# Kernel tuning notes

Hardware: AMD Instinct MI355X
Metric: run time of the kernel (lower is better)

Reference implementation:

```python
import jax, jax.numpy as jnp
import numpy as np

DIM = 1024
NUM_EXPERTS = 4
NUM_HEADS = 16
MLP_RATIO = 4
B, N = 8, 1024
EPS = 1e-5


def layernorm(x, w, b):
    mu = jnp.mean(x, axis=-1, keepdims=True)
    var = jnp.mean(jnp.square(x - mu), axis=-1, keepdims=True)
    return (x - mu) * jax.lax.rsqrt(var + EPS) * w + b


def setup_inputs() -> dict:
    key = jax.random.key(0)
    ks = jax.random.split(key, 6)
    x = jax.random.normal(ks[0], (B, N, DIM), dtype=jnp.float32)
    expert_mask = jax.random.randint(ks[1], (B, N), 0, NUM_EXPERTS)
    expert_probs = jax.random.uniform(ks[2], (B, N), dtype=jnp.float32)
    expand_dim = 3 * DIM + MLP_RATIO * DIM
    expand_weight = jax.random.normal(ks[3], (expand_dim, DIM), dtype=jnp.float32) * 0.02
    mlp_bias = jnp.zeros((MLP_RATIO * DIM,), dtype=jnp.float32)
    contract_weight = jax.random.normal(ks[4], (2 * DIM, MLP_RATIO * DIM + DIM), dtype=jnp.float32) * 0.02
    contract_bias = jnp.zeros((2 * DIM,), dtype=jnp.float32)
    norm1_w = jnp.ones((DIM,), dtype=jnp.float32)
    norm1_b = jnp.zeros((DIM,), dtype=jnp.float32)
    norm2_w = jnp.ones((2 * DIM,), dtype=jnp.float32)
    norm2_b = jnp.zeros((2 * DIM,), dtype=jnp.float32)
    return {"x": x, "expert_probs": expert_probs, "expand_weight": expand_weight,
            "mlp_bias": mlp_bias, "contract_weight": contract_weight,
            "contract_bias": contract_bias, "norm1_w": norm1_w, "norm1_b": norm1_b,
            "norm2_w": norm2_w, "norm2_b": norm2_b, "expert_mask": expert_mask}


def reference(x, expert_probs, expand_weight, mlp_bias, contract_weight,
              contract_bias, norm1_w, norm1_b, norm2_w, norm2_b, expert_mask):
    dim = DIM
    # nested sub-dim per token: expert m uses first dim >> (E-1-m) features
    shift = NUM_EXPERTS - 1 - expert_mask                       # (B, N)
    d_in = dim // jnp.left_shift(1, shift)                      # (B, N)
    in_mask = (jnp.arange(dim)[None, None, :] < d_in[..., None]).astype(x.dtype)

    # fused expand bias: [mlp_bias, qkv_bias(=zeros since qkv_bias=False)]
    input_bias = jnp.concatenate([mlp_bias, jnp.zeros((3 * dim,), x.dtype)], axis=-1)

    xn = layernorm(x, norm1_w, norm1_b) * in_mask               # nested_linear_expand input masking
    y = jnp.einsum('bnd,ed->bne', xn, expand_weight) + input_bias  # (B, N, 7*dim)

    qkv, mlp_hidden = y[..., :3 * dim], y[..., 3 * dim:]
    q = qkv[..., :dim]
    kv = layernorm(qkv[..., dim:], norm2_w, norm2_b)            # (B, N, 2*dim)
    k, v = kv[..., :dim], kv[..., dim:]

    # multi-head attention
    dh = dim // NUM_HEADS
    scale = dh ** -0.5
    b, n = x.shape[0], x.shape[1]
    def heads(t):
        return t.reshape(b, n, NUM_HEADS, dh).transpose(0, 2, 1, 3)
    qh, kh, vh = heads(q), heads(k), heads(v)
    attn = jax.nn.softmax(jnp.einsum('bhqd,bhkd->bhqk', qh, kh) * scale, axis=-1)
    attn_output = jnp.einsum('bhqk,bhkd->bhqd', attn, vh).transpose(0, 2, 1, 3).reshape(b, n, dim)

    # nested_linear_contract: full matmul, then mask outputs beyond (2*dim)>>shift
    concat_in = jnp.concatenate([jax.nn.gelu(mlp_hidden, approximate=False), attn_output], axis=-1)
    cy = jnp.einsum('bnc,oc->bno', concat_in, contract_weight) + contract_bias  # (B, N, 2*dim)
    d_out = (2 * dim) // jnp.left_shift(1, shift)
    out_mask = (jnp.arange(2 * dim)[None, None, :] < d_out[..., None]).astype(x.dtype)
    cy = cy * out_mask + jnp.concatenate([x, x], axis=-1)       # residual.repeat(1,1,2)

    mlp_output, attn_out = cy[..., :dim], cy[..., dim:]
    return attn_out + expert_probs[..., None] * mlp_output
```

## Files before the change

### kernel.cpp

```cpp
#include <hip/hip_runtime.h>
#include <cmath>

#define NT    8192
#define DIM_  1024
#define EXP_  7168
#define CD_   5120
#define OD_   2048
#define MPAD  8704
#define NRT   68

typedef __attribute__((ext_vector_type(8))) short short8;
typedef __attribute__((ext_vector_type(4))) float f32x4;
typedef __attribute__((ext_vector_type(4))) unsigned short ushort4_t;

__device__ __forceinline__ unsigned short f2bf(float f) {
  union { float f; unsigned u; } v; v.f = f;
  return (unsigned short)((v.u + 0x7FFFu + ((v.u >> 16) & 1u)) >> 16);
}
__device__ __forceinline__ float bf2f(unsigned short u) {
  union { unsigned u; float f; } v; v.u = ((unsigned)u) << 16;
  return v.f;
}
__device__ __forceinline__ float fast_gelu(float x) {
  float y = 1.5957691216f * (x + 0.044715f * x * x * x);
  float e = __expf(y);
  float t = 1.f - 2.f * __builtin_amdgcn_rcpf(1.f + e);
  return 0.5f * x * (1.f + t);
}

#define MFMA16(a, b, c) __builtin_amdgcn_mfma_f32_16x16x32_bf16(a, b, c, 0, 0, 0)

__global__ __launch_bounds__(256) void count_experts(const int* __restrict__ em,
                                                     int* __restrict__ blockCnt) {
  __shared__ int h[4];
  int tid = threadIdx.x;
  if (tid < 4) h[tid] = 0;
  __syncthreads();
  atomicAdd(&h[em[blockIdx.x * 256 + tid]], 1);
  __syncthreads();
  if (tid < 4) blockCnt[blockIdx.x * 4 + tid] = h[tid];
}

__global__ void scan_make(const int* __restrict__ blockCnt, int* __restrict__ desc) {
  if (threadIdx.x != 0) return;
  int cnt[4] = {0, 0, 0, 0};
  for (int b = 0; b < 32; b++)
    for (int e = 0; e < 4; e++) cnt[e] += blockCnt[b * 4 + e];
  int base[4]; int acc = 0;
  for (int e = 0; e < 4; e++) { base[e] = acc; acc += ((cnt[e] + 127) >> 7) << 7; }
  for (int e = 0; e < 4; e++) { desc[e] = base[e]; desc[4 + e] = cnt[e]; }
  for (int r = 0; r < NRT; r++) {
    int te = -1;
    for (int e = 0; e < 4; e++) {
      int lo = base[e] >> 7;
      int hi = (base[e] + (((cnt[e] + 127) >> 7) << 7)) >> 7;
      if (r >= lo && r < hi) te = e;
    }
    desc[8 + r] = te;
  }
  int run[4];
  for (int e = 0; e < 4; e++) run[e] = base[e];
  for (int b = 0; b < 32; b++)
    for (int e = 0; e < 4; e++) { desc[76 + b * 4 + e] = run[e]; run[e] += blockCnt[b * 4 + e]; }
}

__global__ __launch_bounds__(256) void fill_perm(int* __restrict__ perm) {
  int i = blockIdx.x * 256 + threadIdx.x;
  if (i < MPAD) perm[i] = -1;
}

__global__ __launch_bounds__(256) void scatter_perm(const int* __restrict__ em,
    const int* __restrict__ desc, int* __restrict__ perm, int* __restrict__ pos) {
  __shared__ int wsum[4][4];
  int tid = threadIdx.x;
  int wv = tid >> 6, ln = tid & 63;
  int t = blockIdx.x * 256 + tid;
  int e = em[t];
  int wrank = 0;
#pragma unroll
  for (int k = 0; k < 4; k++) {
    unsigned long long m = __ballot(e == k);
    if (ln == 0) wsum[wv][k] = __popcll(m);
    if (e == k) wrank = __popcll(m & ((1ull << ln) - 1ull));
  }
  __syncthreads();
  int off = desc[76 + blockIdx.x * 4 + e];
  for (int w = 0; w < wv; w++) off += wsum[w][e];
  int p = off + wrank;
  perm[p] = t;
  pos[t] = p;
}

__global__ __launch_bounds__(256) void cvt_bf16(const float* __restrict__ in,
                                                unsigned short* __restrict__ out, int n) {
  int i = (blockIdx.x * 256 + threadIdx.x) * 4;
  if (i >= n) return;
  float4 v = *(const float4*)(in + i);
  ushort4_t o;
  o[0] = f2bf(v.x); o[1] = f2bf(v.y); o[2] = f2bf(v.z); o[3] = f2bf(v.w);
  *(ushort4_t*)(out + i) = o;
}

__global__ __launch_bounds__(256) void ln1_kernel(const float* __restrict__ x,
    const float* __restrict__ w, const float* __restrict__ b,
    const int* __restrict__ emask, const int* __restrict__ pos,
    unsigned short* __restrict__ xn) {
  int wave = threadIdx.x >> 6, lane = threadIdx.x & 63;
  int t = blockIdx.x * 4 + wave;
  const float* xt = x + (size_t)t * DIM_;
  float4 v[4];
  float s = 0.f, s2 = 0.f;
#pragma unroll
  for (int i = 0; i < 4; i++) {
    v[i] = *(const float4*)(xt + i * 256 + lane * 4);
    s  += v[i].x + v[i].y + v[i].z + v[i].w;
    s2 += v[i].x * v[i].x + v[i].y * v[i].y + v[i].z * v[i].z + v[i].w * v[i].w;
  }
#pragma unroll
  for (int o = 1; o < 64; o <<= 1) { s += __shfl_xor(s, o); s2 += __shfl_xor(s2, o); }
  float mu = s * (1.f / 1024.f);
  float rs = rsqrtf(s2 * (1.f / 1024.f) - mu * mu + 1e-5f);
  int din = 1024 >> (3 - emask[t]);
  unsigned short* ot = xn + (size_t)pos[t] * DIM_;
#pragma unroll
  for (int i = 0; i < 4; i++) {
    int c0 = i * 256 + lane * 4;
    float fv[4] = { v[i].x, v[i].y, v[i].z, v[i].w };
    ushort4_t o;
#pragma unroll
    for (int j = 0; j < 4; j++) {
      int c = c0 + j;
      float val = (c < din) ? (fv[j] - mu) * rs * w[c] + b[c] : 0.f;
      o[j] = f2bf(val);
    }
    *(ushort4_t*)(ot + c0) = o;
  }
}

__global__ __launch_bounds__(256, 3) void gemm_grp1(
    const unsigned short* __restrict__ A, const unsigned short* __restrict__ W,
    const float* __restrict__ bias, const int* __restrict__ tdesc,
    const int* __restrict__ perm, unsigned short* __restrict__ out0,
    unsigned short* __restrict__ out1, unsigned short* __restrict__ out2) {
  __shared__ unsigned short lds[16384];
  unsigned short* As = lds;
  unsigned short* Bs = lds + 8192;
  const int r = blockIdx.y;
  const int e = tdesc[8 + r];
  if (e < 0) return;
  const int ntiles = 4 << e;
  constexpr int KK = 1024;

  const int tid = threadIdx.x;
  const int lane = tid & 63;
  const int wave = tid >> 6;
  const int wm = wave >> 1, wn = wave & 1;
  const int lg = lane >> 4, lr = lane & 15;

  constexpr int CPX = 56 >> 3;
  const int bx = (int)blockIdx.x;
  const int bn = (bx & 7) * CPX + (bx >> 3);
  const int n0 = bn * 128;
  const int m0 = r * 128;

  const int s0g = tid >> 3,        s1g = (256 + tid) >> 3;
  const int lc0 = (tid & 7) ^ (s0g & 7), lc1 = (tid & 7) ^ (s1g & 7);
  const int row0 = 2 * s0g + (lc0 >> 2), kc0 = lc0 & 3;
  const int row1 = 2 * s1g + (lc1 >> 2), kc1 = lc1 & 3;
  const unsigned short* aS0 = A + (size_t)(m0 + row0) * KK + kc0 * 8;
  const unsigned short* aS1 = A + (size_t)(m0 + row1) * KK + kc1 * 8;
  const unsigned short* bS0 = W + (size_t)(n0 + row0) * KK + kc0 * 8;
  const unsigned short* bS1 = W + (size_t)(n0 + row1) * KK + kc1 * 8;

#define GLD(SRC, DST)                                                                \
  __builtin_amdgcn_global_load_lds(                                                  \
      (const __attribute__((address_space(1))) void*)(SRC),                          \
      (__attribute__((address_space(3))) void*)(DST), 16, 0, 0)
#define STAGE(T, SLOT) {                                                             \
    GLD(aS0 + (size_t)(T) * 32, As + (SLOT) * 4096 + tid * 8);                       \
    GLD(aS1 + (size_t)(T) * 32, As + (SLOT) * 4096 + 2048 + tid * 8);                \
    GLD(bS0 + (size_t)(T) * 32, Bs + (SLOT) * 4096 + tid * 8);                       \
    GLD(bS1 + (size_t)(T) * 32, Bs + (SLOT) * 4096 + 2048 + tid * 8);                \
  }

  const int fb = (lr >> 1) * 128 + ((((lr & 1) << 2) + lg) ^ ((lr >> 1) & 7)) * 16;
  const char* apb = (const char*)As + wm * 4096 + fb;
  const char* bpb = (const char*)Bs + wn * 4096 + fb;

  short8 afr[4], bfr[4];
#define LDFRAG(C)                                                                    \
  _Pragma("unroll") for (int mi = 0; mi < 4; mi++)                                   \
    afr[mi] = *(const short8*)(apb + (C) * 8192 + mi * 1024);                        \
  _Pragma("unroll") for (int ni = 0; ni < 4; ni++)                                   \
    bfr[ni] = *(const short8*)(bpb + (C) * 8192 + ni * 1024);

  f32x4 acc[4][4];
  f32x4 zf = { 0.f, 0.f, 0.f, 0.f };
#pragma unroll
  for (int i = 0; i < 4; i++)
#pragma unroll
    for (int j = 0; j < 4; j++) acc[i][j] = zf;

  STAGE(0, 0)
  STAGE(1, 1)
  asm volatile("s_waitcnt vmcnt(4)" ::: "memory");
  __builtin_amdgcn_s_barrier();

#pragma unroll 1
  for (int t = 0; t < ntiles; ++t) {
    const int c = t & 1;
    LDFRAG(c)
    asm volatile("s_waitcnt lgkmcnt(0)" ::: "memory");
    __builtin_amdgcn_sched_barrier(0);
    __builtin_amdgcn_s_barrier();
    const int t2 = (t + 2 < ntiles) ? t + 2 : t;
    STAGE(t2, c)
    __builtin_amdgcn_s_setprio(1);
#pragma unroll
    for (int mi = 0; mi < 4; mi++)
#pragma unroll
      for (int ni = 0; ni < 4; ni++)
        acc[mi][ni] = MFMA16(afr[mi], bfr[ni], acc[mi][ni]);
    __builtin_amdgcn_s_setprio(0);
    asm volatile("s_waitcnt vmcnt(4)" ::: "memory");
    __builtin_amdgcn_s_barrier();
  }
  asm volatile("s_waitcnt vmcnt(0)" ::: "memory");

  const int n0w = n0 + wn * 64;
  auto epi_loop = [&](auto&& body) {
#pragma unroll
    for (int mi = 0; mi < 4; mi++)
#pragma unroll
      for (int ni = 0; ni < 4; ni++)
#pragma unroll
        for (int rr = 0; rr < 4; rr++) {
          int grow = m0 + wm * 64 + mi * 16 + lg * 4 + rr;
          int tk = perm[grow];
          int gcol = n0w + ni * 16 + lr;
          body(tk, gcol, acc[mi][ni][rr]);
        }
  };
  if (n0w < 1024) {
    epi_loop([&](int tk, int gcol, float v) {
      if (tk >= 0) {
        float vv = (v + bias[gcol]) * 0.125f;
        int bb = tk >> 10;
        int n = tk & 1023;
        int h = gcol >> 6;
        int d = gcol & 63;
        out0[(((size_t)(bb * 16 + h) * 1024 + n) << 6) + d] = f2bf(vv);
      }
    });
  } else if (n0w < 3072) {
    epi_loop([&](int tk, int gcol, float v) {
      if (tk >= 0) out1[(size_t)tk * OD_ + (gcol - 1024)] = f2bf(v + bias[gcol]);
    });
  } else {
    const bool hasb = (n0w < 4096);
    epi_loop([&](int tk, int gcol, float v) {
      if (tk >= 0) {
        float vb = v + (hasb ? bias[gcol] : 0.f);
        out2[(size_t)tk * CD_ + (gcol - 3072)] = f2bf(fast_gelu(vb));
      }
    });
  }
#undef GLD
#undef STAGE
#undef LDFRAG
}

__global__ __launch_bounds__(512, 2) void gemm2_8p(
    const unsigned short* __restrict__ A, const unsigned short* __restrict__ W,
    const float* __restrict__ bias, unsigned short* __restrict__ out0) {
  extern __shared__ unsigned short lds[];
  unsigned short* As = lds;
  unsigned short* Bs = lds + 32768;
  constexpr int KK = 5120;
  constexpr int NTILES = KK / 64;
  const int tid = threadIdx.x;
  const int lane = tid & 63;
  const int wave = tid >> 6;
  const int wm = wave >> 2;
  const int wn = wave & 3;
  const int lg = lane >> 4, lr = lane & 15;

  int cpx = (int)gridDim.x >> 3;
  int lid = ((int)blockIdx.x & 7) * cpx + ((int)blockIdx.x >> 3);
  int bm = lid >> 3, bn = lid & 7;
  int m0 = bm * 256, n0 = bn * 256;

  const int srow = tid >> 3;
  const int schunk = (tid & 7) ^ (srow & 7);
  const unsigned short* aSrc = A + (size_t)(m0 + srow) * KK + schunk * 8;
  const unsigned short* bSrc = W + (size_t)(n0 + srow) * KK + schunk * 8;

  const int xor0 = (lg ^ (lr & 7)) * 8;
  const int xor1 = ((4 + lg) ^ (lr & 7)) * 8;
  const unsigned short* ap0 = As + (wm * 64 + lr) * 64 + xor0;
  const unsigned short* ap1 = As + (wm * 64 + lr) * 64 + xor1;
  const unsigned short* bp0 = Bs + (wn * 32 + lr) * 64 + xor0;
  const unsigned short* bp1 = Bs + (wn * 32 + lr) * 64 + xor1;

#define STAGE_A(TT, SLOT, SEG)                                                       \
  __builtin_amdgcn_global_load_lds(                                                  \
    (const __attribute__((address_space(1))) void*)(aSrc +                           \
      (size_t)(SEG) * 64 * KK + (size_t)(TT) * 64),                                  \
    (__attribute__((address_space(3))) void*)(As + (SLOT) * 16384 +                  \
      (SEG) * 4096 + tid * 8), 16, 0, 0)
#define STAGE_B(TT, SLOT, SEG)                                                       \
  __builtin_amdgcn_global_load_lds(                                                  \
    (const __attribute__((address_space(1))) void*)(bSrc +                           \
      (size_t)(SEG) * 64 * KK + (size_t)(TT) * 64),                                  \
    (__attribute__((address_space(3))) void*)(Bs + (SLOT) * 16384 +                  \
      (SEG) * 4096 + tid * 8), 16, 0, 0)

  short8 afr[4][2], bfr[2][2][2];
#define LDFRAG_A(C, QM)                                                              \
  _Pragma("unroll") for (int mi = 0; mi < 4; mi++) {                                 \
    afr[mi][0] = *(const short8*)(ap0 + (C) * 16384 + (QM) * 8192 + mi * 1024);      \
    afr[mi][1] = *(const short8*)(ap1 + (C) * 16384 + (QM) * 8192 + mi * 1024);      \
  }
#define LDFRAG_B(C, QN)                                                              \
  _Pragma("unroll") for (int ni = 0; ni < 2; ni++) {                                 \
    bfr[QN][ni][0] = *(const short8*)(bp0 + (C) * 16384 + (QN) * 8192 + ni * 1024);  \
    bfr[QN][ni][1] = *(const short8*)(bp1 + (C) * 16384 + (QN) * 8192 + ni * 1024);  \
  }
#define DOMFMA(QM, QN)                                                               \
  __builtin_amdgcn_s_setprio(1);                                                     \
  _Pragma("unroll") for (int mi = 0; mi < 4; mi++)                                   \
  _Pragma("unroll") for (int ni = 0; ni < 2; ni++) {                                 \
    acc[(QM) * 4 + mi][(QN) * 2 + ni] =                                              \
        MFMA16(afr[mi][0], bfr[QN][ni][0], acc[(QM) * 4 + mi][(QN) * 2 + ni]);       \
    acc[(QM) * 4 + mi][(QN) * 2 + ni] =                                              \
        MFMA16(afr[mi][1], bfr[QN][ni][1], acc[(QM) * 4 + mi][(QN) * 2 + ni]);       \
  }                                                                                  \
  __builtin_amdgcn_s_setprio(0);

#define SCHED0 __builtin_amdgcn_sched_barrier(0)

#define TILE_BODY(T, C) {                                                            \
    const int tn1 = ((T) + 1 < NTILES) ? (T) + 1 : NTILES - 1;                       \
    const int tn2 = ((T) + 2 < NTILES) ? (T) + 2 : NTILES - 1;                       \
    LDFRAG_A(C, 0); LDFRAG_B(C, 0);                                                  \
    STAGE_B(tn1, (C) ^ 1, 2); STAGE_B(tn1, (C) ^ 1, 3);                              \
    SCHED0;                                                                          \
    __builtin_amdgcn_s_barrier();                                                    \
    asm volatile("s_waitcnt lgkmcnt(0)");                                            \
    SCHED0;                                                                          \
    DOMFMA(0, 0);                                                                    \
    asm volatile("s_waitcnt vmcnt(6)" ::: "memory");                                 \
    __builtin_amdgcn_s_barrier();                                                    \
    LDFRAG_B(C, 1);                                                                  \
    STAGE_A(tn1, (C) ^ 1, 2); STAGE_A(tn1, (C) ^ 1, 3);                              \
    SCHED0;                                                                          \
    __builtin_amdgcn_s_barrier();                                                    \
    asm volatile("s_waitcnt lgkmcnt(0)");                                            \
    SCHED0;                                                                          \
    DOMFMA(0, 1);                                                                    \
    __builtin_amdgcn_s_barrier();                                                    \
    LDFRAG_A(C, 1);                                                                  \
    STAGE_A(tn2, (C), 0); STAGE_A(tn2, (C), 1);                                      \
    SCHED0;                                                                          \
    __builtin_amdgcn_s_barrier();                                                    \
    asm volatile("s_waitcnt lgkmcnt(0)");                                            \
    SCHED0;                                                                          \
    DOMFMA(1, 0);                                                                    \
    __builtin_amdgcn_s_barrier();                                                    \
    STAGE_B(tn2, (C), 0); STAGE_B(tn2, (C), 1);                                      \
    SCHED0;                                                                          \
    __builtin_amdgcn_s_barrier();                                                    \
    DOMFMA(1, 1);                                                                    \
    asm volatile("s_waitcnt vmcnt(8)" ::: "memory");                                 \
    __builtin_amdgcn_s_barrier();                                                    \
  }

  f32x4 acc[8][4];
  f32x4 zf = { 0.f, 0.f, 0.f, 0.f };
#pragma unroll
  for (int i = 0; i < 8; i++)
#pragma unroll
    for (int j = 0; j < 4; j++) acc[i][j] = zf;

  STAGE_A(0, 0, 0); STAGE_A(0, 0, 1); STAGE_A(0, 0, 2); STAGE_A(0, 0, 3);
  STAGE_B(0, 0, 0); STAGE_B(0, 0, 1); STAGE_B(0, 0, 2); STAGE_B(0, 0, 3);
  STAGE_A(1, 1, 0); STAGE_A(1, 1, 1);
  STAGE_B(1, 1, 0); STAGE_B(1, 1, 1);
  asm volatile("s_waitcnt vmcnt(4)" ::: "memory");
  __builtin_amdgcn_s_barrier();

#pragma unroll 1
  for (int tp = 0; tp < NTILES / 2; ++tp) {
    TILE_BODY(2 * tp, 0)
    TILE_BODY(2 * tp + 1, 1)
  }
  asm volatile("s_waitcnt vmcnt(0)" ::: "memory");

#pragma unroll
  for (int mi8 = 0; mi8 < 8; mi8++) {
#pragma unroll
    for (int nj = 0; nj < 4; nj++) {
#pragma unroll
      for (int r = 0; r < 4; r++) {
        int grow = m0 + wm * 64 + (mi8 >> 2) * 128 + (mi8 & 3) * 16 + lg * 4 + r;
        int gcol = n0 + wn * 32 + (nj >> 1) * 128 + (nj & 1) * 16 + lr;
        float v = acc[mi8][nj][r] + bias[gcol];
        out0[(size_t)grow * OD_ + gcol] = f2bf(v);
      }
    }
  }
#undef STAGE_A
#undef STAGE_B
#undef LDFRAG_A
#undef LDFRAG_B
#undef DOMFMA
#undef SCHED0
#undef TILE_BODY
}

__global__ __launch_bounds__(256) void ln2_kernel(const unsigned short* __restrict__ kv,
    const float* __restrict__ w, const float* __restrict__ b,
    unsigned short* __restrict__ kb, unsigned short* __restrict__ vrm) {
  int wave = threadIdx.x >> 6, lane = threadIdx.x & 63;
  int t = blockIdx.x * 4 + wave;
  const unsigned short* p = kv + (size_t)t * OD_;
  float vals[4][8];
  float s = 0.f, s2 = 0.f;
#pragma unroll
  for (int i = 0; i < 4; i++) {
    short8 v = *(const short8*)(p + i * 512 + lane * 8);
#pragma unroll
    for (int j = 0; j < 8; j++) {
      float f = bf2f((unsigned short)v[j]);
      vals[i][j] = f; s += f; s2 += f * f;
    }
  }
#pragma unroll
  for (int o = 1; o < 64; o <<= 1) { s += __shfl_xor(s, o); s2 += __shfl_xor(s2, o); }
  float mu = s * (1.f / 2048.f);
  float rs = rsqrtf(s2 * (1.f / 2048.f) - mu * mu + 1e-5f);
  int bidx = t >> 10, n = t & 1023;
#pragma unroll
  for (int i = 0; i < 4; i++) {
    int c0 = i * 512 + lane * 8;
    short8 o8;
#pragma unroll
    for (int j = 0; j < 8; j++) {
      int c = c0 + j;
      o8[j] = (short)f2bf((vals[i][j] - mu) * rs * w[c] + b[c]);
    }
    if (c0 < 1024) {
      int h = c0 >> 6, d = c0 & 63;
      *(short8*)(kb + (((size_t)(bidx * 16 + h) * 1024 + n) << 6) + d) = o8;
    } else {
      *(short8*)(vrm + (size_t)t * 1024 + (c0 - 1024)) = o8;
    }
  }
}

__global__ __launch_bounds__(256) void transpose_v(const unsigned short* __restrict__ vrm,
                                                   unsigned short* __restrict__ vt) {
  int bh = blockIdx.x >> 4;
  int nblk = (blockIdx.x & 15) * 64;
  int b = bh >> 4, h = bh & 15;
  __shared__ unsigned short tile[64][65];
  int tid = threadIdx.x;
  int i = tid >> 2;
  int d0 = (tid & 3) * 16;
  const unsigned short* src = vrm + ((size_t)(b * 1024 + nblk + i)) * 1024 + h * 64 + d0;
  short8 v0 = *(const short8*)(src);
  short8 v1 = *(const short8*)(src + 8);
#pragma unroll
  for (int j = 0; j < 8; j++) {
    tile[d0 + j][i] = (unsigned short)v0[j];
    tile[d0 + 8 + j][i] = (unsigned short)v1[j];
  }
  __syncthreads();
  int d = tid >> 2;
  int i0 = (tid & 3) * 16;
  unsigned short* dst = vt + ((size_t)bh * 64 + d) * 1024 + nblk + i0;
  short8 o0, o1;
#pragma unroll
  for (int j = 0; j < 8; j++) { o0[j] = (short)tile[d][i0 + j]; o1[j] = (short)tile[d][i0 + 8 + j]; }
  *(short8*)dst = o0;
  *(short8*)(dst + 8) = o1;
}

__global__ __launch_bounds__(256) void attn_kernel(const unsigned short* __restrict__ q,
    const unsigned short* __restrict__ k, const unsigned short* __restrict__ vt,
    unsigned short* __restrict__ concat) {
  int bid = blockIdx.x;
  int bh = (bid & 7) + 8 * ((bid >> 3) & 15);
  int wv = threadIdx.x >> 6;
  int q0 = ((bid >> 7) & 7) * 128 + wv * 32;
  int lane = threadIdx.x & 63;
  int lg = lane >> 4, lr = lane & 15;
  __shared__ unsigned short plds[4][2][512];
  unsigned short* pw = &plds[wv][0][0];
  const unsigned short* qp = q + (size_t)bh * (1024 * 64);
  const unsigned short* kp = k + (size_t)bh * (1024 * 64);
  const unsigned short* vp = vt + (size_t)bh * (64 * 1024);
  short8 qf[2][2];
#pragma unroll
  for (int rb = 0; rb < 2; rb++)
#pragma unroll
    for (int c = 0; c < 2; c++)
      qf[rb][c] = *(const short8*)(qp + (q0 + rb * 16 + lr) * 64 + c * 32 + lg * 8);
  f32x4 zf = { 0.f, 0.f, 0.f, 0.f };
  f32x4 o[2][4];
  float m[2][4], l[2][4];
#pragma unroll
  for (int rb = 0; rb < 2; rb++) {
#pragma unroll
    for (int r = 0; r < 4; r++) { m[rb][r] = -1e30f; l[rb][r] = 0.f; }
#pragma unroll
    for (int nb = 0; nb < 4; nb++) o[rb][nb] = zf;
  }
  const int prd = lr * 32 + (((lg + lr) & 3) << 3);
  const unsigned short* kb0 = kp + (size_t)lr * 64 + lg * 8;
  const unsigned short* kb1 = kp + (size_t)(16 + lr) * 64 + lg * 8;
  const unsigned short* vb0 = vp + (size_t)(lr) * 1024 + lg * 8;
  const unsigned short* vb1 = vp + (size_t)(16 + lr) * 1024 + lg * 8;
  const unsigned short* vb2 = vp + (size_t)(32 + lr) * 1024 + lg * 8;
  const unsigned short* vb3 = vp + (size_t)(48 + lr) * 1024 + lg * 8;

  short8 kc0, kc1, kc2, kc3;
  short8 vc0, vc1, vc2, vc3;
  kc0 = *(const short8*)(kb0);
  kc1 = *(const short8*)(kb0 + 32);
  kc2 = *(const short8*)(kb1);
  kc3 = *(const short8*)(kb1 + 32);

#pragma unroll 1
  for (int kt = 0; kt < 1024; kt += 32) {
    vc0 = *(const short8*)(vb0 + kt);
    vc1 = *(const short8*)(vb1 + kt);
    vc2 = *(const short8*)(vb2 + kt);
    vc3 = *(const short8*)(vb3 + kt);
    asm volatile("s_waitcnt vmcnt(4)" ::: "memory");
    f32x4 s[2][2];
    s[0][0] = zf; s[0][1] = zf; s[1][0] = zf; s[1][1] = zf;
    __builtin_amdgcn_s_setprio(1);
    s[0][0] = MFMA16(qf[0][0], kc0, s[0][0]);
    s[0][0] = MFMA16(qf[0][1], kc1, s[0][0]);
    s[1][0] = MFMA16(qf[1][0], kc0, s[1][0]);
    s[1][0] = MFMA16(qf[1][1], kc1, s[1][0]);
    s[0][1] = MFMA16(qf[0][0], kc2, s[0][1]);
    s[0][1] = MFMA16(qf[0][1], kc3, s[0][1]);
    s[1][1] = MFMA16(qf[1][0], kc2, s[1][1]);
    s[1][1] = MFMA16(qf[1][1], kc3, s[1][1]);
    __builtin_amdgcn_s_setprio(0);
    {
      const size_t ktn = (kt + 32 < 1024) ? (size_t)(kt + 32) : (size_t)kt;
      kc0 = *(const short8*)(kb0 + ktn * 64);
      kc1 = *(const short8*)(kb0 + ktn * 64 + 32);
      kc2 = *(const short8*)(kb1 + ktn * 64);
      kc3 = *(const short8*)(kb1 + ktn * 64 + 32);
    }
#pragma unroll
    for (int rb = 0; rb < 2; rb++) {
      float lmax[4], rsum[4];
#pragma unroll
      for (int r = 0; r < 4; r++) lmax[r] = fmaxf(s[rb][0][r], s[rb][1][r]);
      bool loc = false;
#pragma unroll
      for (int r = 0; r < 4; r++) loc |= (lmax[r] > m[rb][r] + 8.f);
      if (__ballot(loc) != 0ull) {
        float mx[4];
#pragma unroll
        for (int r = 0; r < 4; r++) mx[r] = lmax[r];
#pragma unroll
        for (int ofs = 1; ofs < 16; ofs <<= 1)
#pragma unroll
          for (int r = 0; r < 4; r++) mx[r] = fmaxf(mx[r], __shfl_xor(mx[r], ofs));
#pragma unroll
        for (int r = 0; r < 4; r++) {
          float mn = fmaxf(m[rb][r], mx[r]);
          float al = __expf(m[rb][r] - mn);
          m[rb][r] = mn;
          l[rb][r] *= al;
#pragma unroll
          for (int nb = 0; nb < 4; nb++) o[rb][nb][r] *= al;
        }
      }
#pragma unroll
      for (int r = 0; r < 4; r++) {
        float p0 = __expf(s[rb][0][r] - m[rb][r]);
        float p1 = __expf(s[rb][1][r] - m[rb][r]);
        int q_ = lg * 4 + r;
        pw[rb * 512 + q_ * 32 + ((((lr >> 3) + q_) & 3) << 3) + (lr & 7)] = f2bf(p0);
        pw[rb * 512 + q_ * 32 + (((2 + (lr >> 3) + q_) & 3) << 3) + (lr & 7)] = f2bf(p1);
        rsum[r] = p0 + p1;
      }
#pragma unroll
      for (int ofs = 1; ofs < 16; ofs <<= 1)
#pragma unroll
        for (int r = 0; r < 4; r++) rsum[r] += __shfl_xor(rsum[r], ofs);
#pragma unroll
      for (int r = 0; r < 4; r++) l[rb][r] += rsum[r];
    }
    asm volatile("s_waitcnt lgkmcnt(0)" ::: "memory");
    short8 pf0 = *(const short8*)(pw + prd);
    short8 pf1 = *(const short8*)(pw + 512 + prd);
    asm volatile("s_waitcnt vmcnt(4)" ::: "memory");
    __builtin_amdgcn_s_setprio(1);
    o[0][0] = MFMA16(pf0, vc0, o[0][0]);
    o[1][0] = MFMA16(pf1, vc0, o[1][0]);
    o[0][1] = MFMA16(pf0, vc1, o[0][1]);
    o[1][1] = MFMA16(pf1, vc1, o[1][1]);
    o[0][2] = MFMA16(pf0, vc2, o[0][2]);
    o[1][2] = MFMA16(pf1, vc2, o[1][2]);
    o[0][3] = MFMA16(pf0, vc3, o[0][3]);
    o[1][3] = MFMA16(pf1, vc3, o[1][3]);
    __builtin_amdgcn_s_setprio(0);
  }
  int b = bh >> 4, h = bh & 15;
#pragma unroll
  for (int rb = 0; rb < 2; rb++)
#pragma unroll
    for (int r = 0; r < 4; r++) {
      int n = q0 + rb * 16 + lg * 4 + r;
      size_t t = (size_t)b * 1024 + n;
      float inv = 1.f / l[rb][r];
#pragma unroll
      for (int nb = 0; nb < 4; nb++)
        concat[t * CD_ + 4096 + h * 64 + nb * 16 + lr] = f2bf(o[rb][nb][r] * inv);
    }
}

__global__ __launch_bounds__(256) void final_epi(const unsigned short* __restrict__ cy,
    const float* __restrict__ x, const float* __restrict__ probs,
    const int* __restrict__ emask, float* __restrict__ out) {
  int t = blockIdx.x;
  int c = threadIdx.x * 4;
  int dout = 2048 >> (3 - emask[t]);
  float p = probs[t];
  const unsigned short* cyt = cy + (size_t)t * OD_;
  ushort4_t mv = *(const ushort4_t*)(cyt + c);
  ushort4_t av = *(const ushort4_t*)(cyt + 1024 + c);
  float4 xv = *(const float4*)(x + (size_t)t * 1024 + c);
  float xa[4] = { xv.x, xv.y, xv.z, xv.w };
  float4 o;
  float oa[4];
#pragma unroll
  for (int j = 0; j < 4; j++) {
    float mlp = ((c + j) < dout ? bf2f(mv[j]) : 0.f) + xa[j];
    float att = ((1024 + c + j) < dout ? bf2f(av[j]) : 0.f) + xa[j];
    oa[j] = att + p * mlp;
  }
  o.x = oa[0]; o.y = oa[1]; o.z = oa[2]; o.w = oa[3];
  *(float4*)(out + (size_t)t * 1024 + c) = o;
}

extern "C" void kernel_launch(void* const* d_in, const int* in_sizes, int n_in,
                              void* d_out, int out_size, void* d_ws, size_t ws_size,
                              hipStream_t stream) {
  const float* x        = (const float*)d_in[0];
  const float* probs    = (const float*)d_in[1];
  const float* we       = (const float*)d_in[2];
  const float* mlp_bias = (const float*)d_in[3];
  const float* wc       = (const float*)d_in[4];
  const float* cbias    = (const float*)d_in[5];
  const float* n1w      = (const float*)d_in[6];
  const float* n1b      = (const float*)d_in[7];
  const float* n2w      = (const float*)d_in[8];
  const float* n2b      = (const float*)d_in[9];
  const int*   emask    = (const int*)d_in[10];
  float* out = (float*)d_out;

  char* ws = (char*)d_ws;
  size_t off = 0;
  auto alloc = [&](size_t bytes) {
    char* p = ws + off;
    off += (bytes + 255) & ~(size_t)255;
    return p;
  };
  unsigned short* we_bf = (unsigned short*)alloc((size_t)EXP_ * DIM_ * 2);
  unsigned short* wc_bf = (unsigned short*)alloc((size_t)OD_ * CD_ * 2);
  unsigned short* xn    = (unsigned short*)alloc((size_t)MPAD * DIM_ * 2);
  unsigned short* qb    = (unsigned short*)alloc((size_t)NT * DIM_ * 2);
  unsigned short* kv    = (unsigned short*)alloc((size_t)NT * OD_ * 2);
  unsigned short* kb    = (unsigned short*)alloc((size_t)NT * DIM_ * 2);
  unsigned short* vt    = (unsigned short*)alloc((size_t)NT * DIM_ * 2);
  unsigned short* cc    = (unsigned short*)alloc((size_t)NT * CD_ * 2);
  int* blockCnt         = (int*)alloc(32 * 4 * 4);
  int* desc             = (int*)alloc(256 * 4);
  int* perm             = (int*)alloc(MPAD * 4);
  int* pos              = (int*)alloc(NT * 4);
  unsigned short* vrm = xn;
  unsigned short* cy  = kv;
  if (off > ws_size) return;

  hipFuncSetAttribute((const void*)gemm2_8p,
                      hipFuncAttributeMaxDynamicSharedMemorySize, 131072);

  count_experts<<<32, 256, 0, stream>>>(emask, blockCnt);
  scan_make<<<1, 64, 0, stream>>>(blockCnt, desc);
  fill_perm<<<34, 256, 0, stream>>>(perm);
  scatter_perm<<<32, 256, 0, stream>>>(emask, desc, perm, pos);

  cvt_bf16<<<7168, 256, 0, stream>>>(we, we_bf, EXP_ * DIM_);
  cvt_bf16<<<10240, 256, 0, stream>>>(wc, wc_bf, OD_ * CD_);
  ln1_kernel<<<2048, 256, 0, stream>>>(x, n1w, n1b, emask, pos, xn);
  gemm_grp1<<<dim3(56, NRT), 256, 0, stream>>>(xn, we_bf, mlp_bias, desc,
                                               perm, qb, kv, cc);
  ln2_kernel<<<2048, 256, 0, stream>>>(kv, n2w, n2b, kb, vrm);
  transpose_v<<<2048, 256, 0, stream>>>(vrm, vt);
  attn_kernel<<<1024, 256, 0, stream>>>(qb, kb, vt, cc);
  gemm2_8p<<<256, 512, 131072, stream>>>(cc, wc_bf, cbias, cy);
  final_epi<<<8192, 256, 0, stream>>>(cy, x, probs, emask, out);
}
```

Baseline: 465.2 us.

## Group contract GEMM by expert, skip masked output tiles, and split K

The contract GEMM now walks tokens in expert-grouped order through the permutation array. Each 256-row tile skips output-column tiles beyond the largest d_out of its experts, since those outputs are masked to zero anyway. K is split into two halves written to separate partial buffers, and the bias add plus the partial sum move into final_epi, which reads rows through pos. This removes roughly half of the contract-GEMM FLOPs and adds blocks for occupancy, at the cost of extra partial-buffer traffic in the epilogue and reliance on the workspace reuse of xn/qb/kv regions.

```diff
diff --git a/kernel.cpp b/kernel.cpp
--- a/kernel.cpp
+++ b/kernel.cpp
@@ -272,28 +272,40 @@
 
 __global__ __launch_bounds__(512, 2) void gemm2_8p(
     const unsigned short* __restrict__ A, const unsigned short* __restrict__ W,
-    const float* __restrict__ bias, unsigned short* __restrict__ out0) {
+    const int* __restrict__ tdesc, const int* __restrict__ perm,
+    unsigned short* __restrict__ pk0, unsigned short* __restrict__ pk1) {
   extern __shared__ unsigned short lds[];
   unsigned short* As = lds;
   unsigned short* Bs = lds + 32768;
   constexpr int KK = 5120;
-  constexpr int NTILES = KK / 64;
+  constexpr int NTILES = 40;
+  const int r = blockIdx.y;
+  const int ea = tdesc[8 + 2 * r];
+  const int eb = tdesc[8 + 2 * r + 1];
+  const int emax = (ea > eb) ? ea : eb;
+  if (emax < 0) return;
+  const int bn = ((int)blockIdx.x + r) & 7;
+  if (bn >= (1 << emax)) return;
+  const int k0 = (int)blockIdx.z * 2560;
+
   const int tid = threadIdx.x;
   const int lane = tid & 63;
   const int wave = tid >> 6;
   const int wm = wave >> 2;
   const int wn = wave & 3;
   const int lg = lane >> 4, lr = lane & 15;
-
-  int cpx = (int)gridDim.x >> 3;
-  int lid = ((int)blockIdx.x & 7) * cpx + ((int)blockIdx.x >> 3);
-  int bm = lid >> 3, bn = lid & 7;
-  int m0 = bm * 256, n0 = bn * 256;
+  const int m0 = r * 256, n0 = bn * 256;
 
   const int srow = tid >> 3;
   const int schunk = (tid & 7) ^ (srow & 7);
-  const unsigned short* aSrc = A + (size_t)(m0 + srow) * KK + schunk * 8;
-  const unsigned short* bSrc = W + (size_t)(n0 + srow) * KK + schunk * 8;
+  const unsigned short* aSrcS[4];
+#pragma unroll
+  for (int s4 = 0; s4 < 4; s4++) {
+    int tk = perm[m0 + s4 * 64 + srow];
+    if (tk < 0) tk = 0;
+    aSrcS[s4] = A + (size_t)tk * KK + k0 + schunk * 8;
+  }
+  const unsigned short* bSrc = W + (size_t)(n0 + srow) * KK + k0 + schunk * 8;
 
   const int xor0 = (lg ^ (lr & 7)) * 8;
   const int xor1 = ((4 + lg) ^ (lr & 7)) * 8;
@@ -304,8 +316,8 @@
 
 #define STAGE_A(TT, SLOT, SEG)                                                       \
   __builtin_amdgcn_global_load_lds(                                                  \
-    (const __attribute__((address_space(1))) void*)(aSrc +                           \
-      (size_t)(SEG) * 64 * KK + (size_t)(TT) * 64),                                  \
+    (const __attribute__((address_space(1))) void*)(aSrcS[SEG] +                     \
+      (size_t)(TT) * 64),                                                            \
     (__attribute__((address_space(3))) void*)(As + (SLOT) * 16384 +                  \
       (SEG) * 4096 + tid * 8), 16, 0, 0)
 #define STAGE_B(TT, SLOT, SEG)                                                       \
@@ -396,16 +408,16 @@
   }
   asm volatile("s_waitcnt vmcnt(0)" ::: "memory");
 
+  unsigned short* dst = blockIdx.z ? pk1 : pk0;
 #pragma unroll
   for (int mi8 = 0; mi8 < 8; mi8++) {
 #pragma unroll
     for (int nj = 0; nj < 4; nj++) {
 #pragma unroll
-      for (int r = 0; r < 4; r++) {
-        int grow = m0 + wm * 64 + (mi8 >> 2) * 128 + (mi8 & 3) * 16 + lg * 4 + r;
+      for (int r2 = 0; r2 < 4; r2++) {
+        int grow = m0 + wm * 64 + (mi8 >> 2) * 128 + (mi8 & 3) * 16 + lg * 4 + r2;
         int gcol = n0 + wn * 32 + (nj >> 1) * 128 + (nj & 1) * 16 + lr;
-        float v = acc[mi8][nj][r] + bias[gcol];
-        out0[(size_t)grow * OD_ + gcol] = f2bf(v);
+        dst[(size_t)grow * OD_ + gcol] = f2bf(acc[mi8][nj][r2]);
       }
     }
   }
@@ -628,24 +640,29 @@
     }
 }
 
-__global__ __launch_bounds__(256) void final_epi(const unsigned short* __restrict__ cy,
+__global__ __launch_bounds__(256) void final_epi(const unsigned short* __restrict__ p0,
+    const unsigned short* __restrict__ p1, const float* __restrict__ cbias,
     const float* __restrict__ x, const float* __restrict__ probs,
-    const int* __restrict__ emask, float* __restrict__ out) {
+    const int* __restrict__ emask, const int* __restrict__ pos,
+    float* __restrict__ out) {
   int t = blockIdx.x;
   int c = threadIdx.x * 4;
   int dout = 2048 >> (3 - emask[t]);
   float p = probs[t];
-  const unsigned short* cyt = cy + (size_t)t * OD_;
-  ushort4_t mv = *(const ushort4_t*)(cyt + c);
-  ushort4_t av = *(const ushort4_t*)(cyt + 1024 + c);
+  size_t row = (size_t)pos[t] * OD_;
+  ushort4_t m0v = *(const ushort4_t*)(p0 + row + c);
+  ushort4_t m1v = *(const ushort4_t*)(p1 + row + c);
+  ushort4_t a0v = *(const ushort4_t*)(p0 + row + 1024 + c);
+  ushort4_t a1v = *(const ushort4_t*)(p1 + row + 1024 + c);
   float4 xv = *(const float4*)(x + (size_t)t * 1024 + c);
   float xa[4] = { xv.x, xv.y, xv.z, xv.w };
   float4 o;
   float oa[4];
 #pragma unroll
   for (int j = 0; j < 4; j++) {
-    float mlp = ((c + j) < dout ? bf2f(mv[j]) : 0.f) + xa[j];
-    float att = ((1024 + c + j) < dout ? bf2f(av[j]) : 0.f) + xa[j];
+    float mlp = ((c + j) < dout ? bf2f(m0v[j]) + bf2f(m1v[j]) + cbias[c + j] : 0.f) + xa[j];
+    float att = ((1024 + c + j) < dout ?
+                 bf2f(a0v[j]) + bf2f(a1v[j]) + cbias[1024 + c + j] : 0.f) + xa[j];
     oa[j] = att + p * mlp;
   }
   o.x = oa[0]; o.y = oa[1]; o.z = oa[2]; o.w = oa[3];
@@ -688,7 +705,8 @@
   int* perm             = (int*)alloc(MPAD * 4);
   int* pos              = (int*)alloc(NT * 4);
   unsigned short* vrm = xn;
-  unsigned short* cy  = kv;
+  unsigned short* pk0 = xn;
+  unsigned short* pk1 = xn + (size_t)MPAD * OD_;
   if (off > ws_size) return;
 
   hipFuncSetAttribute((const void*)gemm2_8p,
@@ -707,6 +725,6 @@
   ln2_kernel<<<2048, 256, 0, stream>>>(kv, n2w, n2b, kb, vrm);
   transpose_v<<<2048, 256, 0, stream>>>(vrm, vt);
   attn_kernel<<<1024, 256, 0, stream>>>(qb, kb, vt, cc);
-  gemm2_8p<<<256, 512, 131072, stream>>>(cc, wc_bf, cbias, cy);
-  final_epi<<<8192, 256, 0, stream>>>(cy, x, probs, emask, out);
-}
+  gemm2_8p<<<dim3(8, 34, 2), 512, 131072, stream>>>(cc, wc_bf, desc, perm, pk0, pk1);
+  final_epi<<<8192, 256, 0, stream>>>(pk0, pk1, cbias, x, probs, emask, pos, out);
+}
```

Measured after the change: 468.8 us. About the same (+0.8%).
